# Optimization experiments

Hardware: AMD Instinct MI355X
Metric: run time of the kernel (lower is better)

## Reference

```python
import jax, jax.numpy as jnp
import numpy as np

DIM = 1024
HEADS = 16
HIDDEN = 4096
EPS = 1e-5


def _layernorm(x, g, b):
    mu = jnp.mean(x, axis=-1, keepdims=True)
    var = jnp.mean(jnp.square(x - mu), axis=-1, keepdims=True)
    return (x - mu) * jax.lax.rsqrt(var + EPS) * g + b


def setup_inputs() -> dict:
    key = jax.random.key(0)
    ks = jax.random.split(key, 12)
    B, N, C, Hd = 2, 2048, DIM, HIDDEN
    s = 0.02
    inp = {
        "x": jax.random.normal(ks[0], (B, N, C), dtype=jnp.float32),
        "mask": jax.random.randint(ks[1], (B, N), 0, 2).astype(bool),
        "ln1_g": jnp.ones((C,), jnp.float32),
        "ln1_b": jnp.zeros((C,), jnp.float32),
        "qkv_w": jax.random.normal(ks[2], (3 * C, C), jnp.float32) * s,
        "q_bias": jax.random.normal(ks[3], (C,), jnp.float32) * s,
        "v_bias": jax.random.normal(ks[4], (C,), jnp.float32) * s,
        "proj_w": jax.random.normal(ks[5], (C, C), jnp.float32) * s,
        "proj_b": jnp.zeros((C,), jnp.float32),
        "ln2_g": jnp.ones((C,), jnp.float32),
        "ln2_b": jnp.zeros((C,), jnp.float32),
        "fc1_w": jax.random.normal(ks[6], (Hd, C), jnp.float32) * s,
        "fc1_b": jnp.zeros((Hd,), jnp.float32),
        "fc2_w": jax.random.normal(ks[7], (C, Hd), jnp.float32) * s,
        "fc2_b": jnp.zeros((C,), jnp.float32),
    }
    return inp


def _block(x, mask, ln1_g, ln1_b, qkv_w, q_bias, v_bias, proj_w, proj_b,
           ln2_g, ln2_b, fc1_w, fc1_b, fc2_w, fc2_b):
    B, N, C = x.shape
    H = HEADS
    hd = C // H
    scale = hd ** -0.5

    # --- attention branch ---
    xn = _layernorm(x, ln1_g, ln1_b)
    qkv_bias = jnp.concatenate([q_bias, jnp.zeros_like(v_bias), v_bias])
    qkv = xn @ qkv_w.T + qkv_bias                       # [B,N,3C]
    qkv = qkv.reshape(B, N, 3, H, hd).transpose(2, 0, 3, 1, 4)  # [3,B,H,N,hd]
    q, k, v = qkv[0], qkv[1], qkv[2]
    q = q * scale
    attn = jnp.einsum('bhqd,bhkd->bhqk',
                      q.astype(jnp.float32), k.astype(jnp.float32))
    attn = jnp.where(mask[:, None, None, :], -jnp.inf, attn)
    attn = jax.nn.softmax(attn, axis=-1).astype(x.dtype)
    out = jnp.einsum('bhqk,bhkd->bhqd', attn, v)        # [B,H,N,hd]
    out = out.transpose(0, 2, 1, 3).reshape(B, N, C)
    out = out @ proj_w.T + proj_b
    x = x + out

    # --- MLP branch (Mlp_ returns pre-activation hidden too; norm=Identity) ---
    x2 = _layernorm(x, ln2_g, ln2_b)
    h = x2 @ fc1_w.T + fc1_b                            # [B,N,HIDDEN]
    x_interm = h
    h = jax.nn.gelu(h, approximate=False)
    y = h @ fc2_w.T + fc2_b
    x = x + y
    return x_interm, x


def reference(x, mask, ln1_g, ln1_b, qkv_w, q_bias, v_bias, proj_w, proj_b,
              ln2_g, ln2_b, fc1_w, fc1_b, fc2_w, fc2_b):
    return _block(x, mask, ln1_g, ln1_b, qkv_w, q_bias, v_bias, proj_w, proj_b,
                  ln2_g, ln2_b, fc1_w, fc1_b, fc2_w, fc2_b)
```

## Files before the change

kernel.cpp:

```cpp
#include <hip/hip_runtime.h>
#include <hip/hip_bf16.h>

typedef __attribute__((ext_vector_type(8))) short short8;
typedef __attribute__((ext_vector_type(4))) short short4v;
typedef __attribute__((ext_vector_type(4))) float f32x4;

__device__ inline float bf2f(short s) {
    unsigned u = ((unsigned)(unsigned short)s) << 16;
    float f; __builtin_memcpy(&f, &u, 4); return f;
}
__device__ inline short f2bf(float f) {
    unsigned u; __builtin_memcpy(&u, &f, 4);
    unsigned r = (u + 0x7fffu + ((u >> 16) & 1u)) >> 16;
    return (short)r;
}
__device__ inline float ex2(float x) {
    float r; asm("v_exp_f32 %0, %1" : "=v"(r) : "v"(x)); return r;
}
__device__ inline unsigned cvtpk(float lo, float hi) {
    unsigned r; asm("v_cvt_pk_bf16_f32 %0, %1, %2" : "=v"(r) : "v"(lo), "v"(hi)); return r;
}

#define GLD_LDS16(g, l) __builtin_amdgcn_global_load_lds( \
    (const __attribute__((address_space(1))) void*)(g),   \
    (__attribute__((address_space(3))) void*)(l), 16, 0, 0)

__global__ __launch_bounds__(256) void detect_kernel(const ushort* __restrict__ x,
                                                     const unsigned char* __restrict__ m,
                                                     int* __restrict__ flags) {
    __shared__ int cnt, weirdAny, weird40, nzNon4;
    if (threadIdx.x == 0) { cnt = 0; weirdAny = 0; weird40 = 0; nzNon4 = 0; }
    __syncthreads();
    for (int t = threadIdx.x; t < 512; t += 256) {
        unsigned u = x[2 * t];
        int e = (int)((u >> 7) & 0xFF);
        if (e >= 100 && e <= 130) atomicAdd(&cnt, 1);
    }
    for (int i = threadIdx.x; i < 4096; i += 256) {
        unsigned b = m[i];
        if (b > 1) { atomicOr(&weirdAny, 1); if ((i & 3) == 0) atomicOr(&weird40, 1); }
        if (b != 0 && (i & 3) != 0) atomicOr(&nzNon4, 1);
    }
    __syncthreads();
    if (threadIdx.x == 0) {
        flags[0] = (cnt < 256) ? 1 : 0;
        flags[1] = weirdAny ? (weird40 ? 2 : 3) : (nzNon4 ? 1 : 0);
    }
}

__global__ __launch_bounds__(256) void norm_bf(const void* __restrict__ src,
                                               ushort* __restrict__ dst, int n,
                                               const int* __restrict__ flags) {
    bool f32w = flags[0] != 0;
    int i = (blockIdx.x * 256 + threadIdx.x) * 8;
    int stride = gridDim.x * 256 * 8;
    for (; i < n; i += stride) {
        if (f32w) {
            const float* s = (const float*)src;
            short8 o;
            for (int j = 0; j < 8; j++) o[j] = f2bf(s[i + j]);
            *(short8*)&dst[i] = o;
        } else {
            *(short8*)&dst[i] = *(const short8*)((const ushort*)src + i);
        }
    }
}

__global__ __launch_bounds__(256) void mask_norm(const void* __restrict__ msrc,
                                                 unsigned char* __restrict__ mdst,
                                                 const int* __restrict__ flags) {
    int i = blockIdx.x * 256 + threadIdx.x;
    int enc = flags[1];
    unsigned char v;
    if (enc == 0)      v = (((const int*)msrc)[i] != 0);
    else if (enc == 1) v = (((const unsigned char*)msrc)[i] != 0);
    else if (enc == 2) v = (((const ushort*)msrc)[i] != 0);
    else               v = ((((const unsigned*)msrc)[i] << 1) != 0);
    mdst[i] = v;
}

__global__ __launch_bounds__(256) void ln_kernel(const ushort* __restrict__ x,
                                                 const ushort* __restrict__ g,
                                                 const ushort* __restrict__ b,
                                                 ushort* __restrict__ y) {
    int row = blockIdx.x;
    int tid = threadIdx.x;
    const ushort* xp = x + row * 1024;
    short4v v = *(const short4v*)&xp[tid * 4];
    float f[4]; float s = 0.f, ss = 0.f;
    for (int i = 0; i < 4; i++) { f[i] = bf2f(v[i]); s += f[i]; ss += f[i] * f[i]; }
    for (int o = 1; o < 64; o <<= 1) { s += __shfl_xor(s, o, 64); ss += __shfl_xor(ss, o, 64); }
    __shared__ float sb[8];
    int wave = tid >> 6, lane = tid & 63;
    if (lane == 0) { sb[wave] = s; sb[wave + 4] = ss; }
    __syncthreads();
    s = sb[0] + sb[1] + sb[2] + sb[3];
    ss = sb[4] + sb[5] + sb[6] + sb[7];
    float mu = s * (1.f / 1024.f);
    float var = ss * (1.f / 1024.f) - mu * mu;
    float rstd = rsqrtf(var + 1e-5f);
    short4v gg = *(const short4v*)&g[tid * 4];
    short4v bb = *(const short4v*)&b[tid * 4];
    short4v o;
    for (int i = 0; i < 4; i++) o[i] = f2bf((f[i] - mu) * rstd * bf2f(gg[i]) + bf2f(bb[i]));
    *(short4v*)&y[row * 1024 + tid * 4] = o;
}

template <int EPI>
__device__ __forceinline__ void gemm_body(ushort* SM,
                                          const ushort* __restrict__ A,
                                          const ushort* __restrict__ W,
                                          int K,
                                          const ushort* __restrict__ p0,
                                          const ushort* __restrict__ p1,
                                          void* __restrict__ o0,
                                          ushort* __restrict__ o1,
                                          const int* __restrict__ flags) {
    int tid = threadIdx.x;
    int wave = tid >> 6, lane = tid & 63;
    int wr = wave >> 1, wc = wave & 1;
    int lr = lane & 15, lg = lane >> 4;
    int m0 = blockIdx.x * 128, n0 = blockIdx.y * 128;
    f32x4 acc[4][4];
    for (int i = 0; i < 4; i++) for (int j = 0; j < 4; j++) acc[i][j] = (f32x4){0.f, 0.f, 0.f, 0.f};

    int s0 = wave * 2;
    int srow = lane >> 2;
    int sslot = (lane & 3) ^ ((srow >> 1) & 3);
    const ushort* gA0 = &A[(size_t)(m0 + s0 * 16 + srow) * K + sslot * 8];
    const ushort* gA1 = gA0 + (size_t)16 * K;
    const ushort* gW0 = &W[(size_t)(n0 + s0 * 16 + srow) * K + sslot * 8];
    const ushort* gW1 = gW0 + (size_t)16 * K;

    auto STAGE = [&](int buf, int k0) {
        ushort* lA = &SM[buf * 4096 + s0 * 512];
        ushort* lW = &SM[8192 + buf * 4096 + s0 * 512];
        GLD_LDS16(gA0 + k0, lA);
        GLD_LDS16(gA1 + k0, lA + 512);
        GLD_LDS16(gW0 + k0, lW);
        GLD_LDS16(gW1 + k0, lW + 512);
    };

    STAGE(0, 0);
    __syncthreads();
    int nk = K >> 5;
    int rs = lg ^ ((lr >> 1) & 3);
    for (int t = 0; t < nk; ++t) {
        int cur = t & 1;
        if (t + 1 < nk) STAGE(cur ^ 1, (t + 1) << 5);
        const ushort* Ab = &SM[cur * 4096];
        const ushort* Wb = &SM[8192 + cur * 4096];
        short8 af[4], wf[4];
        for (int mi = 0; mi < 4; mi++) af[mi] = *(const short8*)&Ab[(wr * 64 + mi * 16 + lr) * 32 + rs * 8];
        for (int ni = 0; ni < 4; ni++) wf[ni] = *(const short8*)&Wb[(wc * 64 + ni * 16 + lr) * 32 + rs * 8];
        for (int mi = 0; mi < 4; mi++)
            for (int ni = 0; ni < 4; ni++)
                acc[mi][ni] = __builtin_amdgcn_mfma_f32_16x16x32_bf16(af[mi], wf[ni], acc[mi][ni], 0, 0, 0);
        __syncthreads();
    }

    float* Cs = (float*)SM;
    bool of32 = (EPI == 2 || EPI == 3) ? (flags[0] != 0) : false;
    int r2 = tid >> 3;
    int lc = tid & 7;
    for (int mi = 0; mi < 4; mi++) {
        __syncthreads();
        int rb = wr * 16 + lg * 4;
        for (int ni = 0; ni < 4; ni++) {
            f32x4 v = acc[mi][ni];
            int cl = wc * 64 + ni * 16 + lr;
            for (int rr = 0; rr < 4; rr++) Cs[(rb + rr) * 132 + cl] = v[rr];
        }
        __syncthreads();
        int grow = m0 + mi * 16 + (r2 < 16 ? r2 : 48 + r2);
        if (EPI == 3 && of32) {
            for (int k = 0; k < 4; k++) {
                int c0l = k * 32 + lc * 4;
                int gcol = n0 + c0l;
                f32x4 v;
                for (int j = 0; j < 4; j++)
                    v[j] = Cs[r2 * 132 + c0l + j] + bf2f(p0[gcol + j])
                         + bf2f(p1[(size_t)grow * 1024 + gcol + j]);
                *(f32x4*)&((float*)o0)[16777216 + (size_t)grow * 1024 + gcol] = v;
            }
        } else {
            for (int half = 0; half < 2; half++) {
                int c0l = half * 64 + lc * 8;
                int gcol = n0 + c0l;
                float hv[8];
                for (int j = 0; j < 8; j++) hv[j] = Cs[r2 * 132 + c0l + j];
                short8 o;
                if (EPI == 0) {
                    int part = gcol >> 10, cc = gcol & 1023;
                    if (part == 0)
                        for (int j = 0; j < 8; j++) o[j] = f2bf((hv[j] + bf2f(p0[cc + j])) * 0.18033688f);
                    else if (part == 1)
                        for (int j = 0; j < 8; j++) o[j] = f2bf(hv[j]);
                    else
                        for (int j = 0; j < 8; j++) o[j] = f2bf(hv[j] + bf2f(p1[cc + j]));
                    *(short8*)&((ushort*)o0)[(size_t)grow * 3072 + gcol] = o;
                } else if (EPI == 1) {
                    for (int j = 0; j < 8; j++)
                        o[j] = f2bf(hv[j] + bf2f(p0[gcol + j])
                                  + bf2f(p1[(size_t)grow * 1024 + gcol + j]));
                    *(short8*)&((ushort*)o0)[(size_t)grow * 1024 + gcol] = o;
                } else if (EPI == 2) {
                    float h[8];
                    short8 og;
                    for (int j = 0; j < 8; j++) {
                        h[j] = hv[j] + bf2f(p0[gcol + j]);
                        float ge = 0.5f * h[j] * (1.f + erff(h[j] * 0.70710678118f));
                        og[j] = f2bf(ge);
                    }
                    *(short8*)&o1[(size_t)grow * 4096 + gcol] = og;
                    if (of32) {
                        float* dst = &((float*)o0)[(size_t)grow * 4096 + gcol];
                        *(f32x4*)&dst[0] = (f32x4){h[0], h[1], h[2], h[3]};
                        *(f32x4*)&dst[4] = (f32x4){h[4], h[5], h[6], h[7]};
                    } else {
                        short8 oh;
                        for (int j = 0; j < 8; j++) oh[j] = f2bf(h[j]);
                        *(short8*)&((ushort*)o0)[(size_t)grow * 4096 + gcol] = oh;
                    }
                } else {
                    for (int j = 0; j < 8; j++)
                        o[j] = f2bf(hv[j] + bf2f(p0[gcol + j])
                                  + bf2f(p1[(size_t)grow * 1024 + gcol + j]));
                    *(short8*)&((ushort*)o0)[16777216 + (size_t)grow * 1024 + gcol] = o;
                }
            }
        }
    }
}

#define GEMM_WRAP(NAME, EPI)                                                          \
__global__ __launch_bounds__(256) void NAME(const ushort* __restrict__ A,            \
                                            const ushort* __restrict__ W, int K,     \
                                            const ushort* __restrict__ p0,           \
                                            const ushort* __restrict__ p1,           \
                                            void* __restrict__ o0,                   \
                                            ushort* __restrict__ o1,                 \
                                            const int* __restrict__ flags) {         \
    __shared__ ushort SM[16384];                                                     \
    gemm_body<EPI>(SM, A, W, K, p0, p1, o0, o1, flags);                              \
}

GEMM_WRAP(gemm_qkv, 0)
GEMM_WRAP(gemm_proj, 1)
GEMM_WRAP(gemm_fc1, 2)
GEMM_WRAP(gemm_fc2, 3)

__global__ __launch_bounds__(256) void vtrans_kernel(const ushort* __restrict__ qkv,
                                                     ushort* __restrict__ vT) {
    __shared__ ushort T[64][72];
    int bh = blockIdx.x;
    int b = bh >> 4, h = bh & 15;
    int n0 = blockIdx.y * 64;
    int t = threadIdx.x;
    int r = t >> 2;
    int c0 = (t & 3) * 16;
    const ushort* src = qkv + (size_t)(b * 2048 + n0 + r) * 3072 + 2048 + h * 64 + c0;
    *(short8*)&T[r][c0]     = *(const short8*)&src[0];
    *(short8*)&T[r][c0 + 8] = *(const short8*)&src[8];
    __syncthreads();
    int d = t >> 2;
    int g0 = (t & 3) * 16;
    short8 o0v, o1v;
    for (int j = 0; j < 8; j++) { o0v[j] = T[g0 + j][d]; o1v[j] = T[g0 + 8 + j][d]; }
    ushort* dst = vT + ((size_t)bh * 64 + d) * 2048 + n0 + g0;
    *(short8*)&dst[0] = o0v;
    *(short8*)&dst[8] = o1v;
}

__global__ __launch_bounds__(256) void attn_kernel(const ushort* __restrict__ qkv,
                                                   const ushort* __restrict__ vT,
                                                   const unsigned char* __restrict__ mask,
                                                   ushort* __restrict__ ao) {
    __shared__ ushort Ks[2][4096];
    __shared__ ushort Vs[2][4096];
    __shared__ unsigned Plw[4][544];
    __shared__ unsigned Pmf[1024];

    int tid = threadIdx.x, wave = tid >> 6, lane = tid & 63;
    int bid = (blockIdx.x & 7) * 64 + (blockIdx.x >> 3);
    int g = bid * 4 + wave;
    int b = g >> 10;
    int h = (g >> 6) & 15;
    int qt = g & 63;
    int lr = lane & 15, lg = lane >> 4;

    const ushort* qp = qkv + (size_t)(b * 2048 + qt * 32) * 3072 + h * 64;
    const ushort* kp = qkv + (size_t)(b * 2048) * 3072 + 1024 + h * 64;
    const ushort* vp = vT + ((size_t)(b * 16 + h) * 64) * 2048;
    const unsigned char* mk = mask + b * 2048;

    for (int i = tid; i < 1024; i += 256) {
        unsigned lo = mk[2 * i] ? 0u : 0xFFFFu;
        unsigned hi = mk[2 * i + 1] ? 0u : 0xFFFF0000u;
        Pmf[i] = lo | hi;
    }

    short8 qa[2][2];
    for (int sub = 0; sub < 2; sub++)
        for (int ks = 0; ks < 2; ks++)
            qa[sub][ks] = *(const short8*)&qp[(sub * 16 + lr) * 3072 + ks * 32 + lg * 8];
    short8 ones;
    for (int j = 0; j < 8; j++) ones[j] = (short)0x3F80;

    int srowoff = lane >> 3;
    int sslot = (lane & 7) ^ srowoff;
    int rs0 = lg ^ (lr & 7);
    int rs1 = (4 + lg) ^ (lr & 7);

    f32x4 accT[2][4];
    f32x4 accL[2];
    for (int s = 0; s < 2; s++) {
        accL[s] = (f32x4){0.f, 0.f, 0.f, 0.f};
        for (int i = 0; i < 4; i++) accT[s][i] = (f32x4){0.f, 0.f, 0.f, 0.f};
    }

    auto STAGEKV = [&](int buf, int c0) {
        const ushort* ksrc = kp + (size_t)(c0 + wave * 16 + srowoff) * 3072 + sslot * 8;
        GLD_LDS16(ksrc, &Ks[buf][wave * 1024]);
        GLD_LDS16(ksrc + (size_t)8 * 3072, &Ks[buf][wave * 1024 + 512]);
        const ushort* vsrc = vp + (size_t)(wave * 16 + srowoff) * 2048 + c0 + sslot * 8;
        GLD_LDS16(vsrc, &Vs[buf][wave * 1024]);
        GLD_LDS16(vsrc + (size_t)8 * 2048, &Vs[buf][wave * 1024 + 512]);
    };

    STAGEKV(0, 0);
    __syncthreads();

    for (int it = 0; it < 32; ++it) {
        int c0 = it * 64;
        int cur = it & 1;
        if (it < 31) STAGEKV(cur ^ 1, c0 + 64);

        unsigned mw[4][2];
        for (int t = 0; t < 4; t++) {
            uint2 m2 = *(const uint2*)&Pmf[it * 32 + 8 * t + 2 * lg];
            mw[t][0] = m2.x; mw[t][1] = m2.y;
        }
        f32x4 st[2][4];
        for (int t = 0; t < 4; t++) {
            int row = t * 16 + lr;
            short8 kf0 = *(const short8*)&Ks[cur][row * 64 + rs0 * 8];
            short8 kf1 = *(const short8*)&Ks[cur][row * 64 + rs1 * 8];
            for (int sub = 0; sub < 2; sub++) {
                f32x4 z = (f32x4){0.f, 0.f, 0.f, 0.f};
                z = __builtin_amdgcn_mfma_f32_16x16x32_bf16(kf0, qa[sub][0], z, 0, 0, 0);
                z = __builtin_amdgcn_mfma_f32_16x16x32_bf16(kf1, qa[sub][1], z, 0, 0, 0);
                st[sub][t] = z;
            }
        }
        short8 vf[2][4];
        for (int ks = 0; ks < 2; ks++) {
            int rsk = ks ? rs1 : rs0;
            for (int nt = 0; nt < 4; nt++)
                vf[ks][nt] = *(const short8*)&Vs[cur][(nt * 16 + lr) * 64 + rsk * 8];
        }
        for (int sub = 0; sub < 2; sub++) {
            for (int t = 0; t < 4; t++) {
                for (int rrh = 0; rrh < 2; rrh++) {
                    float plo = ex2(st[sub][t][2 * rrh]);
                    float phi = ex2(st[sub][t][2 * rrh + 1]);
                    unsigned w = cvtpk(plo, phi) & mw[t][rrh];
                    Plw[wave][(8 * t + 2 * lg + rrh) * 17 + lr] = w;
                }
            }
            for (int ks = 0; ks < 2; ks++) {
                unsigned wu[4];
                for (int jj = 0; jj < 4; jj++)
                    wu[jj] = Plw[wave][(16 * ks + 4 * lg + jj) * 17 + lr];
                short8 pf;
                __builtin_memcpy(&pf, wu, 16);
                accL[sub] = __builtin_amdgcn_mfma_f32_16x16x32_bf16(ones, pf, accL[sub], 0, 0, 0);
                for (int nt = 0; nt < 4; nt++)
                    accT[sub][nt] = __builtin_amdgcn_mfma_f32_16x16x32_bf16(vf[ks][nt], pf, accT[sub][nt], 0, 0, 0);
            }
        }
        __syncthreads();
    }

    for (int sub = 0; sub < 2; sub++) {
        float ls = accL[sub][0];
        float inv = (ls > 0.f) ? 1.f / ls : 0.f;
        ushort* op = ao + ((size_t)(b * 2048 + qt * 32 + sub * 16) * 1024) + h * 64;
        for (int nt = 0; nt < 4; nt++) {
            unsigned w0 = cvtpk(accT[sub][nt][0] * inv, accT[sub][nt][1] * inv);
            unsigned w1 = cvtpk(accT[sub][nt][2] * inv, accT[sub][nt][3] * inv);
            uint2 ov; ov.x = w0; ov.y = w1;
            *(uint2*)&op[lr * 1024 + 16 * nt + 4 * lg] = ov;
        }
    }
}

extern "C" void kernel_launch(void* const* d_in, const int* in_sizes, int n_in,
                              void* d_out, int out_size, void* d_ws, size_t ws_size,
                              hipStream_t stream) {
    (void)in_sizes; (void)n_in; (void)out_size; (void)ws_size;

    char* w = (char*)d_ws;
    const size_t MB = 1024 * 1024;
    ushort* xn  = (ushort*)(w + 0 * MB);
    ushort* qkv = (ushort*)(w + 8 * MB);
    ushort* vT  = (ushort*)(w + 32 * MB);
    ushort* x1  = (ushort*)(w + 40 * MB);
    ushort* x2n = (ushort*)(w + 48 * MB);
    ushort* gh  = (ushort*)(w + 8 * MB);
    ushort* x_c    = (ushort*)(w + 56 * MB);
    ushort* qkvw_c = (ushort*)(w + 64 * MB);
    ushort* projw_c= (ushort*)(w + 70 * MB);
    ushort* fc1w_c = (ushort*)(w + 72 * MB);
    ushort* fc2w_c = (ushort*)(w + 80 * MB);
    char* small = w + 88 * MB;
    ushort* ln1g_c = (ushort*)(small + 0 * 4096);
    ushort* ln1b_c = (ushort*)(small + 1 * 4096);
    ushort* qbias_c= (ushort*)(small + 2 * 4096);
    ushort* vbias_c= (ushort*)(small + 3 * 4096);
    ushort* projb_c= (ushort*)(small + 4 * 4096);
    ushort* ln2g_c = (ushort*)(small + 5 * 4096);
    ushort* ln2b_c = (ushort*)(small + 6 * 4096);
    ushort* fc1b_c = (ushort*)(small + 7 * 4096);
    ushort* fc2b_c = (ushort*)(small + 9 * 4096);
    unsigned char* mask_c = (unsigned char*)(small + 10 * 4096);
    int* flags = (int*)(small + 11 * 4096);
    ushort* ao = xn;

    detect_kernel<<<1, 256, 0, stream>>>((const ushort*)d_in[0],
                                         (const unsigned char*)d_in[1], flags);

    auto NB = [&](const void* src, ushort* dst, int n) {
        int blocks = (n / 8 + 255) / 256;
        norm_bf<<<blocks, 256, 0, stream>>>(src, dst, n, flags);
    };
    NB(d_in[0],  x_c,     4194304);
    NB(d_in[2],  ln1g_c,  1024);
    NB(d_in[3],  ln1b_c,  1024);
    NB(d_in[4],  qkvw_c,  3145728);
    NB(d_in[5],  qbias_c, 1024);
    NB(d_in[6],  vbias_c, 1024);
    NB(d_in[7],  projw_c, 1048576);
    NB(d_in[8],  projb_c, 1024);
    NB(d_in[9],  ln2g_c,  1024);
    NB(d_in[10], ln2b_c,  1024);
    NB(d_in[11], fc1w_c,  4194304);
    NB(d_in[12], fc1b_c,  4096);
    NB(d_in[13], fc2w_c,  4194304);
    NB(d_in[14], fc2b_c,  1024);
    mask_norm<<<16, 256, 0, stream>>>(d_in[1], mask_c, flags);

    ln_kernel<<<4096, 256, 0, stream>>>(x_c, ln1g_c, ln1b_c, xn);
    gemm_qkv<<<dim3(32, 24), 256, 0, stream>>>(xn, qkvw_c, 1024, qbias_c, vbias_c, qkv, nullptr, flags);
    vtrans_kernel<<<dim3(32, 32), 256, 0, stream>>>(qkv, vT);
    attn_kernel<<<512, 256, 0, stream>>>(qkv, vT, mask_c, ao);
    gemm_proj<<<dim3(32, 8), 256, 0, stream>>>(ao, projw_c, 1024, projb_c, x_c, x1, nullptr, flags);
    ln_kernel<<<4096, 256, 0, stream>>>(x1, ln2g_c, ln2b_c, x2n);
    gemm_fc1<<<dim3(32, 32), 256, 0, stream>>>(x2n, fc1w_c, 1024, fc1b_c, nullptr, d_out, gh, flags);
    gemm_fc2<<<dim3(32, 8), 256, 0, stream>>>(gh, fc2w_c, 4096, fc2b_c, x1, d_out, nullptr, flags);
}
```

Before: 307.0 us.

## Fuse input conversion launches, use wave-per-row layernorm, per-wave GEMM epilogue

Replaces the fifteen separate conversion and mask launches with one prep kernel that dispatches on block index, which removes launch overhead. The layernorm now handles one row per wave with 16 elements per lane and no shared-memory reduction or block barrier. The GEMM epilogue stages each wave's tile in its own shared-memory slice, so the block-wide syncs per row group are gone and residual loads are vectorized. The trade-off is more complex dispatch logic in prep_kernel and a reworked fp32 output path that carries some correctness risk.

Result: slower. 549.2 us (+78.9%).

```diff
diff --git a/kernel.cpp b/kernel.cpp
--- a/kernel.cpp
+++ b/kernel.cpp
@@ -48,62 +48,92 @@
     }
 }
 
-__global__ __launch_bounds__(256) void norm_bf(const void* __restrict__ src,
-                                               ushort* __restrict__ dst, int n,
-                                               const int* __restrict__ flags) {
+__global__ __launch_bounds__(256) void prep_kernel(
+    const void* __restrict__ xs, const void* __restrict__ ms,
+    const void* __restrict__ ln1g, const void* __restrict__ ln1b,
+    const void* __restrict__ qkvw, const void* __restrict__ qb,
+    const void* __restrict__ vb, const void* __restrict__ pw,
+    const void* __restrict__ pb, const void* __restrict__ ln2g,
+    const void* __restrict__ ln2b, const void* __restrict__ f1w,
+    const void* __restrict__ f1b, const void* __restrict__ f2w,
+    const void* __restrict__ f2b,
+    char* __restrict__ w, const int* __restrict__ flags) {
     bool f32w = flags[0] != 0;
-    int i = (blockIdx.x * 256 + threadIdx.x) * 8;
-    int stride = gridDim.x * 256 * 8;
-    for (; i < n; i += stride) {
+    const size_t MB = 1024 * 1024;
+    int bid = blockIdx.x, tid = threadIdx.x;
+    char* small = w + 88 * MB;
+    auto cvt8 = [&](const void* src, ushort* dst, int i) {
         if (f32w) {
-            const float* s = (const float*)src;
+            const float* s = (const float*)src + i;
             short8 o;
-            for (int j = 0; j < 8; j++) o[j] = f2bf(s[i + j]);
+            for (int j = 0; j < 8; j++) o[j] = f2bf(s[j]);
             *(short8*)&dst[i] = o;
         } else {
             *(short8*)&dst[i] = *(const short8*)((const ushort*)src + i);
         }
-    }
-}
-
-__global__ __launch_bounds__(256) void mask_norm(const void* __restrict__ msrc,
-                                                 unsigned char* __restrict__ mdst,
-                                                 const int* __restrict__ flags) {
-    int i = blockIdx.x * 256 + threadIdx.x;
-    int enc = flags[1];
-    unsigned char v;
-    if (enc == 0)      v = (((const int*)msrc)[i] != 0);
-    else if (enc == 1) v = (((const unsigned char*)msrc)[i] != 0);
-    else if (enc == 2) v = (((const ushort*)msrc)[i] != 0);
-    else               v = ((((const unsigned*)msrc)[i] << 1) != 0);
-    mdst[i] = v;
+    };
+    if (bid < 2048)       cvt8(xs,   (ushort*)(w + 56 * MB), (bid * 256 + tid) * 8);
+    else if (bid < 3584)  cvt8(qkvw, (ushort*)(w + 64 * MB), ((bid - 2048) * 256 + tid) * 8);
+    else if (bid < 4096)  cvt8(pw,   (ushort*)(w + 70 * MB), ((bid - 3584) * 256 + tid) * 8);
+    else if (bid < 6144)  cvt8(f1w,  (ushort*)(w + 72 * MB), ((bid - 4096) * 256 + tid) * 8);
+    else if (bid < 8192)  cvt8(f2w,  (ushort*)(w + 80 * MB), ((bid - 6144) * 256 + tid) * 8);
+    else if (bid < 8198) {
+        int e = (bid - 8192) * 2048 + tid * 8;
+        const void* src; ushort* dst; int off;
+        if (e < 7168) {
+            int t = e >> 10; off = e & 1023;
+            const void* s0;
+            if (t == 0) s0 = ln1g; else if (t == 1) s0 = ln1b; else if (t == 2) s0 = qb;
+            else if (t == 3) s0 = vb; else if (t == 4) s0 = pb; else if (t == 5) s0 = ln2g;
+            else s0 = ln2b;
+            src = s0; dst = (ushort*)(small + t * 4096);
+        } else if (e < 8192) { src = f2b; off = e - 7168; dst = (ushort*)(small + 9 * 4096); }
+        else                 { src = f1b; off = e - 8192; dst = (ushort*)(small + 7 * 4096); }
+        cvt8(src, dst, off);
+    } else {
+        int enc = flags[1];
+        unsigned char* md = (unsigned char*)(small + 10 * 4096);
+        int i0 = (bid - 8198) * 2048 + tid * 8;
+        for (int j = 0; j < 8; j++) {
+            int i = i0 + j;
+            unsigned char v;
+            if (enc == 0)      v = (((const int*)ms)[i] != 0);
+            else if (enc == 1) v = (((const unsigned char*)ms)[i] != 0);
+            else if (enc == 2) v = (((const ushort*)ms)[i] != 0);
+            else               v = ((((const unsigned*)ms)[i] << 1) != 0);
+            md[i] = v;
+        }
+    }
 }
 
 __global__ __launch_bounds__(256) void ln_kernel(const ushort* __restrict__ x,
                                                  const ushort* __restrict__ g,
                                                  const ushort* __restrict__ b,
                                                  ushort* __restrict__ y) {
-    int row = blockIdx.x;
-    int tid = threadIdx.x;
-    const ushort* xp = x + row * 1024;
-    short4v v = *(const short4v*)&xp[tid * 4];
-    float f[4]; float s = 0.f, ss = 0.f;
-    for (int i = 0; i < 4; i++) { f[i] = bf2f(v[i]); s += f[i]; ss += f[i] * f[i]; }
+    int wave = threadIdx.x >> 6, lane = threadIdx.x & 63;
+    int row = blockIdx.x * 4 + wave;
+    const ushort* xp = x + (size_t)row * 1024 + lane * 16;
+    short8 v0 = *(const short8*)xp;
+    short8 v1 = *(const short8*)(xp + 8);
+    float f[16]; float s = 0.f, ss = 0.f;
+    for (int i = 0; i < 8; i++) { f[i] = bf2f(v0[i]); f[i + 8] = bf2f(v1[i]); }
+    for (int i = 0; i < 16; i++) { s += f[i]; ss += f[i] * f[i]; }
     for (int o = 1; o < 64; o <<= 1) { s += __shfl_xor(s, o, 64); ss += __shfl_xor(ss, o, 64); }
-    __shared__ float sb[8];
-    int wave = tid >> 6, lane = tid & 63;
-    if (lane == 0) { sb[wave] = s; sb[wave + 4] = ss; }
-    __syncthreads();
-    s = sb[0] + sb[1] + sb[2] + sb[3];
-    ss = sb[4] + sb[5] + sb[6] + sb[7];
     float mu = s * (1.f / 1024.f);
     float var = ss * (1.f / 1024.f) - mu * mu;
     float rstd = rsqrtf(var + 1e-5f);
-    short4v gg = *(const short4v*)&g[tid * 4];
-    short4v bb = *(const short4v*)&b[tid * 4];
-    short4v o;
-    for (int i = 0; i < 4; i++) o[i] = f2bf((f[i] - mu) * rstd * bf2f(gg[i]) + bf2f(bb[i]));
-    *(short4v*)&y[row * 1024 + tid * 4] = o;
+    short8 g0 = *(const short8*)&g[lane * 16];
+    short8 g1 = *(const short8*)&g[lane * 16 + 8];
+    short8 b0 = *(const short8*)&b[lane * 16];
+    short8 b1 = *(const short8*)&b[lane * 16 + 8];
+    short8 o0v, o1v;
+    for (int i = 0; i < 8; i++) {
+        o0v[i] = f2bf((f[i] - mu) * rstd * bf2f(g0[i]) + bf2f(b0[i]));
+        o1v[i] = f2bf((f[i + 8] - mu) * rstd * bf2f(g1[i]) + bf2f(b1[i]));
+    }
+    ushort* yp = y + (size_t)row * 1024 + lane * 16;
+    *(short8*)yp = o0v;
+    *(short8*)(yp + 8) = o1v;
 }
 
 template <int EPI>
@@ -159,74 +189,78 @@
         __syncthreads();
     }
 
-    float* Cs = (float*)SM;
+    float* Csw = (float*)SM + wave * 1088;
     bool of32 = (EPI == 2 || EPI == 3) ? (flags[0] != 0) : false;
-    int r2 = tid >> 3;
-    int lc = tid & 7;
+    int r8 = lane >> 3;
+    int c8 = (lane & 7) * 8;
     for (int mi = 0; mi < 4; mi++) {
-        __syncthreads();
-        int rb = wr * 16 + lg * 4;
         for (int ni = 0; ni < 4; ni++) {
             f32x4 v = acc[mi][ni];
-            int cl = wc * 64 + ni * 16 + lr;
-            for (int rr = 0; rr < 4; rr++) Cs[(rb + rr) * 132 + cl] = v[rr];
-        }
-        __syncthreads();
-        int grow = m0 + mi * 16 + (r2 < 16 ? r2 : 48 + r2);
-        if (EPI == 3 && of32) {
-            for (int k = 0; k < 4; k++) {
-                int c0l = k * 32 + lc * 4;
-                int gcol = n0 + c0l;
-                f32x4 v;
-                for (int j = 0; j < 4; j++)
-                    v[j] = Cs[r2 * 132 + c0l + j] + bf2f(p0[gcol + j])
-                         + bf2f(p1[(size_t)grow * 1024 + gcol + j]);
-                *(f32x4*)&((float*)o0)[16777216 + (size_t)grow * 1024 + gcol] = v;
+            int cl = ni * 16 + lr;
+            for (int rr = 0; rr < 4; rr++) Csw[(lg * 4 + rr) * 68 + cl] = v[rr];
+        }
+        for (int rg = 0; rg < 2; rg++) {
+            int r = rg * 8 + r8;
+            int grow = m0 + wr * 64 + mi * 16 + r;
+            int gcol = n0 + wc * 64 + c8;
+            float hv[8];
+            *(f32x4*)&hv[0] = *(f32x4*)&Csw[r * 68 + c8];
+            *(f32x4*)&hv[4] = *(f32x4*)&Csw[r * 68 + c8 + 4];
+            if (EPI == 0) {
+                int part = gcol >> 10, cc = gcol & 1023;
+                short8 o;
+                if (part == 0)
+                    for (int j = 0; j < 8; j++) o[j] = f2bf((hv[j] + bf2f(p0[cc + j])) * 0.18033688f);
+                else if (part == 1)
+                    for (int j = 0; j < 8; j++) o[j] = f2bf(hv[j]);
+                else
+                    for (int j = 0; j < 8; j++) o[j] = f2bf(hv[j] + bf2f(p1[cc + j]));
+                *(short8*)&((ushort*)o0)[(size_t)grow * 3072 + gcol] = o;
+            } else if (EPI == 1) {
+                short8 r0 = *(const short8*)&p1[(size_t)grow * 1024 + gcol];
+                short8 o;
+                for (int j = 0; j < 8; j++)
+                    o[j] = f2bf(hv[j] + bf2f(p0[gcol + j]) + bf2f(r0[j]));
+                *(short8*)&((ushort*)o0)[(size_t)grow * 1024 + gcol] = o;
+            } else if (EPI == 2) {
+                float h8[8]; short8 og;
+                for (int j = 0; j < 8; j++) {
+                    h8[j] = hv[j] + bf2f(p0[gcol + j]);
+                    float ge = 0.5f * h8[j] * (1.f + erff(h8[j] * 0.70710678118f));
+                    og[j] = f2bf(ge);
+                }
+                *(short8*)&o1[(size_t)grow * 4096 + gcol] = og;
+                if (!of32) {
+                    short8 oh;
+                    for (int j = 0; j < 8; j++) oh[j] = f2bf(h8[j]);
+                    *(short8*)&((ushort*)o0)[(size_t)grow * 4096 + gcol] = oh;
+                }
+            } else {
+                if (!of32) {
+                    short8 r0 = *(const short8*)&p1[(size_t)grow * 1024 + gcol];
+                    short8 o;
+                    for (int j = 0; j < 8; j++)
+                        o[j] = f2bf(hv[j] + bf2f(p0[gcol + j]) + bf2f(r0[j]));
+                    *(short8*)&((ushort*)o0)[16777216 + (size_t)grow * 1024 + gcol] = o;
+                }
             }
-        } else {
-            for (int half = 0; half < 2; half++) {
-                int c0l = half * 64 + lc * 8;
-                int gcol = n0 + c0l;
-                float hv[8];
-                for (int j = 0; j < 8; j++) hv[j] = Cs[r2 * 132 + c0l + j];
-                short8 o;
-                if (EPI == 0) {
-                    int part = gcol >> 10, cc = gcol & 1023;
-                    if (part == 0)
-                        for (int j = 0; j < 8; j++) o[j] = f2bf((hv[j] + bf2f(p0[cc + j])) * 0.18033688f);
-                    else if (part == 1)
-                        for (int j = 0; j < 8; j++) o[j] = f2bf(hv[j]);
-                    else
-                        for (int j = 0; j < 8; j++) o[j] = f2bf(hv[j] + bf2f(p1[cc + j]));
-                    *(short8*)&((ushort*)o0)[(size_t)grow * 3072 + gcol] = o;
-                } else if (EPI == 1) {
-                    for (int j = 0; j < 8; j++)
-                        o[j] = f2bf(hv[j] + bf2f(p0[gcol + j])
-                                  + bf2f(p1[(size_t)grow * 1024 + gcol + j]));
-                    *(short8*)&((ushort*)o0)[(size_t)grow * 1024 + gcol] = o;
-                } else if (EPI == 2) {
-                    float h[8];
-                    short8 og;
-                    for (int j = 0; j < 8; j++) {
-                        h[j] = hv[j] + bf2f(p0[gcol + j]);
-                        float ge = 0.5f * h[j] * (1.f + erff(h[j] * 0.70710678118f));
-                        og[j] = f2bf(ge);
+        }
+        if ((EPI == 2 || EPI == 3) && of32) {
+            int c4 = (lane & 7) * 4;
+            for (int rg = 0; rg < 2; rg++) {
+                int r = rg * 8 + r8;
+                int grow = m0 + wr * 64 + mi * 16 + r;
+                for (int ch = 0; ch < 2; ch++) {
+                    int gcol = n0 + wc * 64 + ch * 32 + c4;
+                    f32x4 v = *(f32x4*)&Csw[r * 68 + ch * 32 + c4];
+                    if (EPI == 2) {
+                        for (int j = 0; j < 4; j++) v[j] += bf2f(p0[gcol + j]);
+                        *(f32x4*)&((float*)o0)[(size_t)grow * 4096 + gcol] = v;
+                    } else {
+                        short4v r0 = *(const short4v*)&p1[(size_t)grow * 1024 + gcol];
+                        for (int j = 0; j < 4; j++) v[j] += bf2f(p0[gcol + j]) + bf2f(r0[j]);
+                        *(f32x4*)&((float*)o0)[16777216 + (size_t)grow * 1024 + gcol] = v;
                     }
-                    *(short8*)&o1[(size_t)grow * 4096 + gcol] = og;
-                    if (of32) {
-                        float* dst = &((float*)o0)[(size_t)grow * 4096 + gcol];
-                        *(f32x4*)&dst[0] = (f32x4){h[0], h[1], h[2], h[3]};
-                        *(f32x4*)&dst[4] = (f32x4){h[4], h[5], h[6], h[7]};
-                    } else {
-                        short8 oh;
-                        for (int j = 0; j < 8; j++) oh[j] = f2bf(h[j]);
-                        *(short8*)&((ushort*)o0)[(size_t)grow * 4096 + gcol] = oh;
-                    }
-                } else {
-                    for (int j = 0; j < 8; j++)
-                        o[j] = f2bf(hv[j] + bf2f(p0[gcol + j])
-                                  + bf2f(p1[(size_t)grow * 1024 + gcol + j]));
-                    *(short8*)&((ushort*)o0)[16777216 + (size_t)grow * 1024 + gcol] = o;
                 }
             }
         }
@@ -429,33 +463,17 @@
 
     detect_kernel<<<1, 256, 0, stream>>>((const ushort*)d_in[0],
                                          (const unsigned char*)d_in[1], flags);
-
-    auto NB = [&](const void* src, ushort* dst, int n) {
-        int blocks = (n / 8 + 255) / 256;
-        norm_bf<<<blocks, 256, 0, stream>>>(src, dst, n, flags);
-    };
-    NB(d_in[0],  x_c,     4194304);
-    NB(d_in[2],  ln1g_c,  1024);
-    NB(d_in[3],  ln1b_c,  1024);
-    NB(d_in[4],  qkvw_c,  3145728);
-    NB(d_in[5],  qbias_c, 1024);
-    NB(d_in[6],  vbias_c, 1024);
-    NB(d_in[7],  projw_c, 1048576);
-    NB(d_in[8],  projb_c, 1024);
-    NB(d_in[9],  ln2g_c,  1024);
-    NB(d_in[10], ln2b_c,  1024);
-    NB(d_in[11], fc1w_c,  4194304);
-    NB(d_in[12], fc1b_c,  4096);
-    NB(d_in[13], fc2w_c,  4194304);
-    NB(d_in[14], fc2b_c,  1024);
-    mask_norm<<<16, 256, 0, stream>>>(d_in[1], mask_c, flags);
-
-    ln_kernel<<<4096, 256, 0, stream>>>(x_c, ln1g_c, ln1b_c, xn);
+    prep_kernel<<<8200, 256, 0, stream>>>(d_in[0], d_in[1], d_in[2], d_in[3], d_in[4],
+                                          d_in[5], d_in[6], d_in[7], d_in[8], d_in[9],
+                                          d_in[10], d_in[11], d_in[12], d_in[13], d_in[14],
+                                          w, flags);
+
+    ln_kernel<<<1024, 256, 0, stream>>>(x_c, ln1g_c, ln1b_c, xn);
     gemm_qkv<<<dim3(32, 24), 256, 0, stream>>>(xn, qkvw_c, 1024, qbias_c, vbias_c, qkv, nullptr, flags);
     vtrans_kernel<<<dim3(32, 32), 256, 0, stream>>>(qkv, vT);
     attn_kernel<<<512, 256, 0, stream>>>(qkv, vT, mask_c, ao);
     gemm_proj<<<dim3(32, 8), 256, 0, stream>>>(ao, projw_c, 1024, projb_c, x_c, x1, nullptr, flags);
-    ln_kernel<<<4096, 256, 0, stream>>>(x1, ln2g_c, ln2b_c, x2n);
+    ln_kernel<<<1024, 256, 0, stream>>>(x1, ln2g_c, ln2b_c, x2n);
     gemm_fc1<<<dim3(32, 32), 256, 0, stream>>>(x2n, fc1w_c, 1024, fc1b_c, nullptr, d_out, gh, flags);
     gemm_fc2<<<dim3(32, 8), 256, 0, stream>>>(gh, fc2w_c, 4096, fc2b_c, x1, d_out, nullptr, flags);
 }
```
